# Kernel optimization log

Hardware: AMD Instinct MI355X
Metric: run time of the kernel (lower is better)

## Reference

```python
import jax, jax.numpy as jnp
import numpy as np

GROUPS = 2
EPS = 1e-5


def channel_shuffle(x, groups=2):
    b, c, h, w = x.shape
    x = x.reshape(b, groups, c // groups, h, w)
    x = jnp.transpose(x, (0, 2, 1, 3, 4))
    return x.reshape(b, c, h, w)


def binarize_weight(w):
    # w: (O, I/g, k, k). scaling_factor = mean |w| over (in,kh,kw), detached.
    scale = jax.lax.stop_gradient(jnp.mean(jnp.abs(w), axis=(1, 2, 3), keepdims=True))
    bw = scale * jnp.sign(w)
    cl = jnp.clip(w, -1.0, 1.0)
    # STE: forward value = bw, gradient flows through clamp
    return jax.lax.stop_gradient(bw) - jax.lax.stop_gradient(cl) + cl


@jax.custom_vjp
def bin_act(x):
    return jnp.sign(x)


def _bin_act_fwd(x):
    return jnp.sign(x), x


def _bin_act_bwd(x, g):
    scale = jnp.where((x >= 1.0) | (x <= -1.0), 0.01, 1.0)
    return (g * scale,)


bin_act.defvjp(_bin_act_fwd, _bin_act_bwd)


def grouped_bin_conv(x, w, pad):
    return jax.lax.conv_general_dilated(
        x, binarize_weight(w), window_strides=(1, 1),
        padding=[(pad, pad), (pad, pad)],
        dimension_numbers=('NCHW', 'OIHW', 'NCHW'),
        feature_group_count=GROUPS)


def batchnorm(x, gamma, beta):
    # training-mode BN: biased batch statistics over (N,H,W)
    mu = jnp.mean(x, axis=(0, 2, 3), keepdims=True)
    var = jnp.mean((x - mu) ** 2, axis=(0, 2, 3), keepdims=True)
    xn = (x - mu) * jax.lax.rsqrt(var + EPS)
    return xn * gamma[None, :, None, None] + beta[None, :, None, None]


def add_bias(x, b):
    return x + b[None, :, None, None]


def prelu(x, a):
    return jnp.where(x >= 0, x, a[None, :, None, None] * x)


def setup_inputs() -> dict:
    key = jax.random.key(0)
    ks = jax.random.split(key, 4)
    C, half = 256, 128
    x = jax.random.normal(ks[0], (32, C, 56, 56), dtype=jnp.float32)
    # two BinaryConvs (64,128,3,3) stacked -> grouped (128,128,3,3)
    w3 = jax.random.uniform(ks[1], (half, C // GROUPS, 3, 3), dtype=jnp.float32) * 0.001
    w1 = jax.random.uniform(ks[2], (half, C // GROUPS, 1, 1), dtype=jnp.float32) * 0.001
    z = jnp.zeros((C,), jnp.float32)
    return {
        'x': x, 'w3': w3, 'w1': w1,
        'b1': z, 'g1': jnp.ones((half,), jnp.float32), 'be1': jnp.zeros((half,), jnp.float32),
        'b2_1': z, 'a2': jnp.full((C,), 0.25, jnp.float32), 'b2_2': z,
        'b3_1': z, 'g3': jnp.ones((half,), jnp.float32), 'be3': jnp.zeros((half,), jnp.float32),
        'b4_1': z, 'a4': jnp.full((C,), 0.25, jnp.float32), 'b4_2': z,
    }


def reference(x, w3, w1, b1, g1, be1, b2_1, a2, b2_2, b3_1, g3, be3, b4_1, a4, b4_2):
    half = w3.shape[0]  # out_channel // 2 = 128
    x = channel_shuffle(x, GROUPS)
    x1 = bin_act(add_bias(x, b1))
    x1 = batchnorm(grouped_bin_conv(x1, w3, pad=1), g1, be1)
    x1_res = x[:, half:]
    x1 = x1 + x[:, :half]
    x2 = jnp.concatenate([x1, x1_res], axis=1)
    x2 = add_bias(prelu(add_bias(x2, b2_1), a2), b2_2)
    x2 = add_bias(x2, b3_1)
    x3 = bin_act(x2)
    x3 = batchnorm(grouped_bin_conv(x3, w1, pad=0), g3, be3)
    x3_res = x2[:, half:]
    x3 = x3 + x2[:, :half]
    x4 = jnp.concatenate([x3, x3_res], axis=1)
    x5 = add_bias(prelu(add_bias(x4, b4_1), a4), b4_2)
    return x5
```

## Files before the change

### kernel.cpp

```cpp
#include <hip/hip_runtime.h>
#include <stdint.h>

typedef unsigned short ushort_t;
typedef unsigned int uint_t;
typedef _Float16 half_t;

typedef float  float4_t __attribute__((ext_vector_type(4)));
typedef float  float2_t __attribute__((ext_vector_type(2)));
typedef _Float16 half4_t __attribute__((ext_vector_type(4)));
typedef _Float16 half2_t __attribute__((ext_vector_type(2)));
typedef uint_t uint4_t  __attribute__((ext_vector_type(4)));

#define B_N 32
#define C_N 256
#define HALF_N 128
#define H_N 56
#define W_N 56
#define HW_N 3136
#define NPIX (B_N * HW_N)
#define EPS_D 1e-5
#define W3S 40
#define PWS 16

__global__ void prep_kernel(const float* __restrict__ w3, const float* __restrict__ w1,
                            uint_t* __restrict__ wbits3, uint_t* __restrict__ wbits1,
                            uint_t* __restrict__ popcw3,
                            double* __restrict__ scale3, double* __restrict__ scale1,
                            double* __restrict__ sums1, double* __restrict__ sums2,
                            uint_t* __restrict__ oflags) {
    __shared__ double red[128];
    __shared__ int ipw[2][9];
    __shared__ int flsh[2];
    int t = threadIdx.x;
    int blk = blockIdx.x;
    int lane = t & 63;
    int wv = t >> 6;
    if (blk == 0) {
        sums1[t] = 0.0; sums1[128 + t] = 0.0;
        sums2[t] = 0.0; sums2[128 + t] = 0.0;
    }
    if (blk < 128) {
        int o = blk;
        double acc = 0.0;
        int anynp = 0;
        #pragma unroll
        for (int j = 0; j < 9; ++j) {
            float v = w3[o * 1152 + t * 9 + j];
            acc += fabs((double)v);
            anynp |= (v <= 0.f) ? 1 : 0;
            unsigned long long b = __ballot(v > 0.f);
            if (lane == 0) {
                wbits3[o * W3S + j * 4 + wv * 2 + 0] = (uint_t)b;
                wbits3[o * W3S + j * 4 + wv * 2 + 1] = (uint_t)(b >> 32);
                ipw[wv][j] = __popcll(b);
            }
        }
        unsigned long long m = __ballot(anynp != 0);
        if (lane == 0) flsh[wv] = (m != 0ull) ? 1 : 0;
        red[t] = acc; __syncthreads();
        for (int s = 64; s > 0; s >>= 1) { if (t < s) red[t] += red[t + s]; __syncthreads(); }
        if (t == 0) { scale3[o] = red[0] / 1152.0; oflags[o] = (uint_t)(flsh[0] | flsh[1]); }
        if (t < 9) popcw3[o * PWS + t] = (uint_t)(ipw[0][t] + ipw[1][t]);
    } else {
        int o = blk - 128;
        float v = w1[o * 128 + t];
        unsigned long long b = __ballot(v > 0.f);
        unsigned long long m = __ballot(v <= 0.f);
        if (lane == 0) {
            wbits1[o * 8 + wv * 2 + 0] = (uint_t)b;
            wbits1[o * 8 + wv * 2 + 1] = (uint_t)(b >> 32);
            flsh[wv] = (m != 0ull) ? 1 : 0;
        }
        red[t] = fabs((double)v); __syncthreads();
        for (int s = 64; s > 0; s >>= 1) { if (t < s) red[t] += red[t + s]; __syncthreads(); }
        if (t == 0) { scale1[o] = red[0] / 128.0; oflags[128 + o] = (uint_t)(flsh[0] | flsh[1]); }
    }
}

__global__ __launch_bounds__(256) void sign1_kernel(const float* __restrict__ x,
                                                    const float* __restrict__ b1,
                                                    uint_t* __restrict__ vb,
                                                    const uint_t* __restrict__ oflags,
                                                    uint_t* __restrict__ fin) {
    __shared__ int fl[4];
    int t = threadIdx.x;
    if (blockIdx.x == 0 && blockIdx.y == 0) {
        int lane = t & 63, wv4 = t >> 6;
        uint_t f = oflags[t];
        unsigned long long m = __ballot(f != 0u);
        if (lane == 0) fl[wv4] = (m != 0ull) ? 1 : 0;
        __syncthreads();
        if (t == 0) { fin[0] = (uint_t)(fl[0] | fl[1]); fin[1] = (uint_t)(fl[2] | fl[3]); }
    }
    int p = blockIdx.x * 1024 + t * 4;
    int cb = blockIdx.y * 32;
    int b = p / HW_N;
    int hw = p - b * HW_N;
    const float* xb = x + (size_t)b * C_N * HW_N + hw;
    uint_t w0 = 0, w1 = 0, w2 = 0, w3 = 0;
    #pragma unroll
    for (int j = 0; j < 32; ++j) {
        int c = cb + j;
        int src = ((c & 1) << 7) + (c >> 1);
        float4_t xv = *(const float4_t*)(xb + (size_t)src * HW_N);
        double bc = (double)b1[c];
        if ((double)xv[0] + bc > 0.0) w0 |= (1u << j);
        if ((double)xv[1] + bc > 0.0) w1 |= (1u << j);
        if ((double)xv[2] + bc > 0.0) w2 |= (1u << j);
        if ((double)xv[3] + bc > 0.0) w3 |= (1u << j);
    }
    uint4_t o4; o4[0] = w0; o4[1] = w1; o4[2] = w2; o4[3] = w3;
    *(uint4_t*)(vb + (size_t)(cb >> 5) * NPIX + p) = o4;
}

__global__ __launch_bounds__(256) void conv3_kernel(const uint_t* __restrict__ vb,
                                                    const uint_t* __restrict__ wbits3,
                                                    const uint_t* __restrict__ popcw3,
                                                    half_t* __restrict__ yh,
                                                    double* __restrict__ sums,
                                                    const uint_t* __restrict__ fin) {
    __shared__ short dlds[32][258];
    __shared__ int partS[8][32];
    __shared__ int partS2[8][32];
    int t = threadIdx.x;
    int lane = t & 63;
    int wv = t >> 6;
    bool fast = (fin[0] == 0u);
    int yb = blockIdx.y;
    if (fast && (yb & 1)) return;
    int g = yb >> 1;
    int oh = yb & 1;
    int o0 = g * 64 + oh * 32;
    int p = blockIdx.x * 256 + t;
    int hw = p % HW_N;
    int h = hw / W_N;
    int w = hw - h * W_N;
    const uint_t* vbase = vb + (size_t)g * 4 * NPIX;

    uint_t v[9][4];
    int inv[9];
    int nvalid = 0;
    #pragma unroll
    for (int j = 0; j < 9; ++j) {
        int kh = j / 3 - 1, kw = j - (j / 3) * 3 - 1;
        int hh = h + kh, ww = w + kw;
        bool valid = (hh >= 0) && (hh < H_N) && (ww >= 0) && (ww < W_N);
        inv[j] = valid ? 0 : 1;
        nvalid += valid ? 1 : 0;
        int off = p + kh * W_N + kw;
        #pragma unroll
        for (int q = 0; q < 4; ++q)
            v[j][q] = valid ? vbase[(size_t)q * NPIX + off] : 0u;
    }
    int base = 128 * nvalid;

    if (fast) {
        int P = 0;
        #pragma unroll
        for (int j = 0; j < 9; ++j)
            #pragma unroll
            for (int q = 0; q < 4; ++q)
                P += __popc(v[j][q]);
        int dot = 2 * P - base;
        yh[(size_t)o0 * NPIX + p] = (half_t)(float)dot;
        int s = dot, s2 = dot * dot;
        #pragma unroll
        for (int off = 32; off > 0; off >>= 1) {
            s  += __shfl_xor(s, off);
            s2 += __shfl_xor(s2, off);
        }
        if (lane == 0) { partS[0][wv] = s; partS2[0][wv] = s2; }
        __syncthreads();
        if (t == 0) {
            partS[1][0]  = partS[0][0] + partS[0][1] + partS[0][2] + partS[0][3];
            partS2[1][0] = partS2[0][0] + partS2[0][1] + partS2[0][2] + partS2[0][3];
        }
        __syncthreads();
        if (t < 64) {
            atomicAdd(&sums[o0 + t], (double)partS[1][0]);
            atomicAdd(&sums[128 + o0 + t], (double)partS2[1][0]);
        }
        return;
    }

    half_t* yrow = yh + (size_t)o0 * NPIX + p;
    for (int oi = 0; oi < 32; ++oi) {
        const uint_t* wo = wbits3 + (size_t)(o0 + oi) * W3S;
        const uint_t* pw = popcw3 + (size_t)(o0 + oi) * PWS;
        int acc = 0;
        #pragma unroll
        for (int j = 0; j < 9; ++j)
            #pragma unroll
            for (int q = 0; q < 4; ++q)
                acc += __popc(v[j][q] ^ wo[j * 4 + q]);
        int corr = 0;
        #pragma unroll
        for (int j = 0; j < 9; ++j) corr += inv[j] * (int)pw[j];
        int dot = base - 2 * (acc - corr);
        yrow[(size_t)oi * NPIX] = (half_t)(float)dot;
        dlds[oi][t] = (short)dot;
    }
    __syncthreads();
    {
        int o = t & 31, seg = t >> 5;
        const int* r32 = (const int*)(&dlds[o][seg * 32]);
        int S = 0, S2 = 0;
        #pragma unroll
        for (int j = 0; j < 16; ++j) {
            int pr = r32[j];
            int d0 = (int)(short)(pr & 0xffff);
            int d1 = pr >> 16;
            S += d0 + d1; S2 += d0 * d0 + d1 * d1;
        }
        partS[seg][o] = S; partS2[seg][o] = S2;
    }
    __syncthreads();
    if (t < 32) {
        int S = 0, S2 = 0;
        #pragma unroll
        for (int s8 = 0; s8 < 8; ++s8) { S += partS[s8][t]; S2 += partS2[s8][t]; }
        int c = o0 + t;
        atomicAdd(&sums[c], (double)S);
        atomicAdd(&sums[128 + c], (double)S2);
    }
}

__device__ __forceinline__ void coef_entry(const double* __restrict__ sums,
                                           const double* __restrict__ scale,
                                           const float* __restrict__ gamma,
                                           const float* __restrict__ beta,
                                           int c, double* coefL) {
    double M = (double)NPIX;
    double mean = sums[c] / M;
    double var = sums[128 + c] / M - mean * mean;
    double s = scale[c];
    double r = 1.0 / sqrt(s * s * var + EPS_D);
    double g = (double)gamma[c];
    coefL[c] = s * r * g;
    coefL[128 + c] = (double)beta[c] - s * mean * r * g;
}

__device__ __forceinline__ void coef_entry_f(const double* __restrict__ sums,
                                             const double* __restrict__ scale,
                                             const float* __restrict__ gamma,
                                             const float* __restrict__ beta,
                                             int c, float* cf) {
    double M = (double)NPIX;
    double mean = sums[c] / M;
    double var = sums[128 + c] / M - mean * mean;
    double s = scale[c];
    double r = 1.0 / sqrt(s * s * var + EPS_D);
    double g = (double)gamma[c];
    cf[c] = (float)(s * r * g);
    cf[128 + c] = (float)((double)beta[c] - s * mean * r * g);
}

__device__ __forceinline__ double x2_val(double xs, double K, bool hasy,
                                         const double* coef1, int c,
                                         const float* __restrict__ b2_1, const float* __restrict__ a2,
                                         const float* __restrict__ b2_2, const float* __restrict__ b3_1) {
    int ci = c & 127;
    double t = hasy ? (coef1[ci] * K + coef1[128 + ci] + xs) : xs;
    t += (double)b2_1[c];
    double a = (double)a2[c];
    t = (t >= 0.0) ? t : a * t;
    t += (double)b2_2[c];
    t += (double)b3_1[c];
    return t;
}

__global__ __launch_bounds__(128) void x2c1_kernel(
        const float* __restrict__ x, const half_t* __restrict__ y1h,
        const double* __restrict__ sums1, const double* __restrict__ scale3,
        const float* __restrict__ g1, const float* __restrict__ be1,
        const float* __restrict__ b2_1, const float* __restrict__ a2,
        const float* __restrict__ b2_2, const float* __restrict__ b3_1,
        const uint_t* __restrict__ wbits1,
        half_t* __restrict__ y3h, double* __restrict__ sums2,
        const float* __restrict__ b4_1, const float* __restrict__ a4,
        const float* __restrict__ b4_2, float* __restrict__ out,
        const uint_t* __restrict__ fin) {
    __shared__ double coefL[256];
    __shared__ short dst[32][258];
    __shared__ int partS[4][32];
    __shared__ int partS2[4][32];
    int t = threadIdx.x;
    int lane = t & 63;
    int wv = t >> 6;
    int g = blockIdx.y;
    bool fast3 = (fin[0] == 0u);
    bool fast1 = (fin[1] == 0u);
    if (g == 0) coef_entry(sums1, scale3, g1, be1, t, coefL);
    __syncthreads();

    int p = blockIdx.x * 256 + t * 2;
    int b = p / HW_N;
    int hw = p - b * HW_N;
    const float* xb = x + (size_t)b * C_N * HW_N + hw;

    uint_t q0 = 0, q1 = 0, q2 = 0, q3 = 0;
    uint_t r0 = 0, r1 = 0, r2 = 0, r3 = 0;
    if (g == 0) {
        if (fast3) {
            half2_t k0  = *(const half2_t*)(y1h + p);
            half2_t k64 = *(const half2_t*)(y1h + (size_t)64 * NPIX + p);
            double K0a = (double)(float)k0[0],  K0b = (double)(float)k0[1];
            double K6a = (double)(float)k64[0], K6b = (double)(float)k64[1];
            #pragma unroll
            for (int wq = 0; wq < 4; ++wq) {
                uint_t ba = 0, bb = 0;
                double Ka = (wq < 2) ? K0a : K6a;
                double Kb = (wq < 2) ? K0b : K6b;
                #pragma unroll
                for (int j = 0; j < 32; ++j) {
                    int c = wq * 32 + j;
                    int src = ((c & 1) << 7) + (c >> 1);
                    float2_t xv = *(const float2_t*)(xb + (size_t)src * HW_N);
                    double va = x2_val((double)xv[0], Ka, true, coefL, c, b2_1, a2, b2_2, b3_1);
                    double vb_ = x2_val((double)xv[1], Kb, true, coefL, c, b2_1, a2, b2_2, b3_1);
                    ba |= (va > 0.0) ? (1u << j) : 0u;
                    bb |= (vb_ > 0.0) ? (1u << j) : 0u;
                }
                if (wq == 0) { q0 = ba; r0 = bb; } else if (wq == 1) { q1 = ba; r1 = bb; }
                else if (wq == 2) { q2 = ba; r2 = bb; } else { q3 = ba; r3 = bb; }
            }
        } else {
            #pragma unroll
            for (int wq = 0; wq < 4; ++wq) {
                uint_t ba = 0, bb = 0;
                #pragma unroll
                for (int j = 0; j < 32; ++j) {
                    int c = wq * 32 + j;
                    int src = ((c & 1) << 7) + (c >> 1);
                    float2_t xv = *(const float2_t*)(xb + (size_t)src * HW_N);
                    half2_t kv = *(const half2_t*)(y1h + (size_t)c * NPIX + p);
                    double va = x2_val((double)xv[0], (double)(float)kv[0], true, coefL, c, b2_1, a2, b2_2, b3_1);
                    double vb_ = x2_val((double)xv[1], (double)(float)kv[1], true, coefL, c, b2_1, a2, b2_2, b3_1);
                    ba |= (va > 0.0) ? (1u << j) : 0u;
                    bb |= (vb_ > 0.0) ? (1u << j) : 0u;
                }
                if (wq == 0) { q0 = ba; r0 = bb; } else if (wq == 1) { q1 = ba; r1 = bb; }
                else if (wq == 2) { q2 = ba; r2 = bb; } else { q3 = ba; r3 = bb; }
            }
        }
    } else {
        #pragma unroll
        for (int wq = 0; wq < 4; ++wq) {
            uint_t ba = 0, bb = 0;
            #pragma unroll
            for (int j = 0; j < 32; ++j) {
                int c = 128 + wq * 32 + j;
                int src = ((c & 1) << 7) + (c >> 1);
                float2_t xv = *(const float2_t*)(xb + (size_t)src * HW_N);
                double va = x2_val((double)xv[0], 0.0, false, coefL, c, b2_1, a2, b2_2, b3_1);
                double vb_ = x2_val((double)xv[1], 0.0, false, coefL, c, b2_1, a2, b2_2, b3_1);
                ba |= (va > 0.0) ? (1u << j) : 0u;
                bb |= (vb_ > 0.0) ? (1u << j) : 0u;
                float b41c = b4_1[c], a4c = a4[c], b42c = b4_2[c];
                float f0 = (float)va + b41c;
                f0 = (f0 >= 0.f) ? f0 : a4c * f0;
                f0 += b42c;
                float f1 = (float)vb_ + b41c;
                f1 = (f1 >= 0.f) ? f1 : a4c * f1;
                f1 += b42c;
                float2_t ov; ov[0] = f0; ov[1] = f1;
                *(float2_t*)(out + ((size_t)b * C_N + c) * HW_N + hw) = ov;
            }
            if (wq == 0) { q0 = ba; r0 = bb; } else if (wq == 1) { q1 = ba; r1 = bb; }
            else if (wq == 2) { q2 = ba; r2 = bb; } else { q3 = ba; r3 = bb; }
        }
    }

    int obase = g * 64;
    if (fast1) {
        int P0 = __popc(q0) + __popc(q1) + __popc(q2) + __popc(q3);
        int P1 = __popc(r0) + __popc(r1) + __popc(r2) + __popc(r3);
        int d0 = 2 * P0 - 128, d1 = 2 * P1 - 128;
        half2_t yv; yv[0] = (half_t)(float)d0; yv[1] = (half_t)(float)d1;
        *(half2_t*)(y3h + (size_t)obase * NPIX + p) = yv;
        int s = d0 + d1, s2 = d0 * d0 + d1 * d1;
        #pragma unroll
        for (int off = 32; off > 0; off >>= 1) {
            s  += __shfl_xor(s, off);
            s2 += __shfl_xor(s2, off);
        }
        if (lane == 0) { partS[0][wv] = s; partS2[0][wv] = s2; }
        __syncthreads();
        if (t == 0) {
            partS[1][0]  = partS[0][0] + partS[0][1];
            partS2[1][0] = partS2[0][0] + partS2[0][1];
        }
        __syncthreads();
        if (t < 64) {
            atomicAdd(&sums2[obase + t], (double)partS[1][0]);
            atomicAdd(&sums2[128 + obase + t], (double)partS2[1][0]);
        }
        return;
    }

    #pragma unroll
    for (int ch = 0; ch < 2; ++ch) {
        #pragma unroll
        for (int oi = 0; oi < 32; ++oi) {
            int o = obase + ch * 32 + oi;
            const uint_t* wo = wbits1 + (size_t)o * 8;
            int a0 = __popc(q0 ^ wo[0]) + __popc(q1 ^ wo[1])
                   + __popc(q2 ^ wo[2]) + __popc(q3 ^ wo[3]);
            int a1 = __popc(r0 ^ wo[0]) + __popc(r1 ^ wo[1])
                   + __popc(r2 ^ wo[2]) + __popc(r3 ^ wo[3]);
            int d0 = 128 - 2 * a0, d1 = 128 - 2 * a1;
            half2_t yv; yv[0] = (half_t)(float)d0; yv[1] = (half_t)(float)d1;
            *(half2_t*)(y3h + (size_t)o * NPIX + p) = yv;
            *(int*)&dst[oi][t * 2] = (d0 & 0xffff) | (d1 << 16);
        }
        __syncthreads();
        {
            int o = t & 31, seg = t >> 5;
            const int* r32 = (const int*)(&dst[o][seg * 64]);
            int S = 0, S2 = 0;
            #pragma unroll
            for (int j = 0; j < 32; ++j) {
                int pr = r32[j];
                int e0 = (int)(short)(pr & 0xffff);
                int e1 = pr >> 16;
                S += e0 + e1; S2 += e0 * e0 + e1 * e1;
            }
            partS[seg][o] = S; partS2[seg][o] = S2;
        }
        __syncthreads();
        if (t < 32) {
            int S  = partS[0][t] + partS[1][t] + partS[2][t] + partS[3][t];
            int S2 = partS2[0][t] + partS2[1][t] + partS2[2][t] + partS2[3][t];
            int c = obase + ch * 32 + t;
            atomicAdd(&sums2[c], (double)S);
            atomicAdd(&sums2[128 + c], (double)S2);
        }
        __syncthreads();
    }
}

__global__ __launch_bounds__(256) void out_kernel(
        const float* __restrict__ x, const half_t* __restrict__ y1h,
        const half_t* __restrict__ y3h,
        const double* __restrict__ sums1, const double* __restrict__ scale3,
        const float* __restrict__ g1, const float* __restrict__ be1,
        const double* __restrict__ sums2, const double* __restrict__ scale1,
        const float* __restrict__ g3, const float* __restrict__ be3,
        const float* __restrict__ b2_1, const float* __restrict__ a2,
        const float* __restrict__ b2_2, const float* __restrict__ b3_1,
        const float* __restrict__ b4_1, const float* __restrict__ a4,
        const float* __restrict__ b4_2, float* __restrict__ out,
        const uint_t* __restrict__ fin) {
    __shared__ float c1f[256];
    __shared__ float c3f[256];
    int t = threadIdx.x;
    if (t < 128) coef_entry_f(sums1, scale3, g1, be1, t, c1f);
    else coef_entry_f(sums2, scale1, g3, be3, t - 128, c3f);
    __syncthreads();
    int c = blockIdx.y;
    int src = ((c & 1) << 7) + (c >> 1);
    int y1slice = (fin[0] == 0u) ? ((c < 64) ? 0 : 64) : c;
    int y3slice = (fin[1] == 0u) ? ((c < 64) ? 0 : 64) : c;
    float b21 = b2_1[c], aa2v = a2[c], b23 = b2_2[c] + b3_1[c];
    float b41 = b4_1[c], aa4v = a4[c], b42 = b4_2[c];
    float c1 = c1f[c], c1b = c1f[128 + c];
    float c3 = c3f[c], c3b = c3f[128 + c];
    const half_t* y1p = y1h + (size_t)y1slice * NPIX;
    const half_t* y3p = y3h + (size_t)y3slice * NPIX;
    #pragma unroll
    for (int i = 0; i < 2; ++i) {
        int p = blockIdx.x * 2048 + i * 1024 + t * 4;
        int b = p / HW_N;
        int hw = p - b * HW_N;
        float4_t xs = *(const float4_t*)(x + ((size_t)b * C_N + src) * HW_N + hw);
        half4_t y1v = *(const half4_t*)(y1p + p);
        half4_t y3v = *(const half4_t*)(y3p + p);
        float4_t ov;
        #pragma unroll
        for (int k = 0; k < 4; ++k) {
            float v = fmaf(c1, (float)y1v[k], c1b) + xs[k];
            v += b21;
            v = (v >= 0.f) ? v : aa2v * v;
            v += b23;
            float t2 = v;
            v = fmaf(c3, (float)y3v[k], c3b) + t2;
            v += b41;
            v = (v >= 0.f) ? v : aa4v * v;
            v += b42;
            ov[k] = v;
        }
        *(float4_t*)(out + ((size_t)b * C_N + c) * HW_N + hw) = ov;
    }
}

extern "C" void kernel_launch(void* const* d_in, const int* in_sizes, int n_in,
                              void* d_out, int out_size, void* d_ws, size_t ws_size,
                              hipStream_t stream) {
    const float* x    = (const float*)d_in[0];
    const float* w3   = (const float*)d_in[1];
    const float* w1   = (const float*)d_in[2];
    const float* b1   = (const float*)d_in[3];
    const float* g1   = (const float*)d_in[4];
    const float* be1  = (const float*)d_in[5];
    const float* b2_1 = (const float*)d_in[6];
    const float* a2   = (const float*)d_in[7];
    const float* b2_2 = (const float*)d_in[8];
    const float* b3_1 = (const float*)d_in[9];
    const float* g3   = (const float*)d_in[10];
    const float* be3  = (const float*)d_in[11];
    const float* b4_1 = (const float*)d_in[12];
    const float* a4   = (const float*)d_in[13];
    const float* b4_2 = (const float*)d_in[14];

    char* ws = (char*)d_ws;
    half_t* y1h    = (half_t*)(ws + 0);
    half_t* y3h    = (half_t*)(ws + 25690112);
    uint_t* wbits3 = (uint_t*)(ws + 51380224);
    uint_t* wbits1 = (uint_t*)(ws + 51400704);
    uint_t* popcw3 = (uint_t*)(ws + 51404800);
    double* scale3 = (double*)(ws + 51412992);
    double* scale1 = (double*)(ws + 51414016);
    double* sums1  = (double*)(ws + 51415040);
    double* sums2  = (double*)(ws + 51417088);
    uint_t* oflags = (uint_t*)(ws + 51419136);
    uint_t* fin    = (uint_t*)(ws + 51420160);

    uint_t* vb1 = (uint_t*)((char*)d_out + 0);
    float*  outp = (float*)d_out;

    prep_kernel<<<256, 128, 0, stream>>>(w3, w1, wbits3, wbits1, popcw3,
                                         scale3, scale1, sums1, sums2, oflags);
    sign1_kernel<<<dim3(NPIX / 1024, 8), 256, 0, stream>>>(x, b1, vb1, oflags, fin);
    conv3_kernel<<<dim3(NPIX / 256, 4), 256, 0, stream>>>(vb1, wbits3, popcw3, y1h, sums1, fin);
    x2c1_kernel<<<dim3(NPIX / 256, 2), 128, 0, stream>>>(x, y1h, sums1, scale3, g1, be1,
                                                         b2_1, a2, b2_2, b3_1,
                                                         wbits1, y3h, sums2,
                                                         b4_1, a4, b4_2, outp, fin);
    out_kernel<<<dim3(NPIX / 2048, 128), 256, 0, stream>>>(x, y1h, y3h,
                                                           sums1, scale3, g1, be1,
                                                           sums2, scale1, g3, be3,
                                                           b2_1, a2, b2_2, b3_1,
                                                           b4_1, a4, b4_2, outp, fin);
}
```

Baseline: 288.0 us.

## Halve per-thread pixel work in sign and x2c1 kernels, split channels across threads

sign1_kernel now handles two pixels per thread with float2 loads, doubling the grid. x2c1_kernel processes one pixel per thread and splits the 128 input channels between two thread halves, exchanging the bit words through shared memory, using 256 threads and twice as many blocks. The aim is more parallelism and latency hiding in these bandwidth-bound kernels. In exchange, global accesses become narrower scalar loads and stores, and the kernel adds a shared-memory exchange and an extra barrier.

```diff
diff --git a/kernel.cpp b/kernel.cpp
--- a/kernel.cpp
+++ b/kernel.cpp
@@ -10,6 +10,7 @@
 typedef _Float16 half4_t __attribute__((ext_vector_type(4)));
 typedef _Float16 half2_t __attribute__((ext_vector_type(2)));
 typedef uint_t uint4_t  __attribute__((ext_vector_type(4)));
+typedef uint_t uint2_t  __attribute__((ext_vector_type(2)));
 
 #define B_N 32
 #define C_N 256
@@ -92,25 +93,23 @@
         __syncthreads();
         if (t == 0) { fin[0] = (uint_t)(fl[0] | fl[1]); fin[1] = (uint_t)(fl[2] | fl[3]); }
     }
-    int p = blockIdx.x * 1024 + t * 4;
+    int p = blockIdx.x * 512 + t * 2;
     int cb = blockIdx.y * 32;
     int b = p / HW_N;
     int hw = p - b * HW_N;
     const float* xb = x + (size_t)b * C_N * HW_N + hw;
-    uint_t w0 = 0, w1 = 0, w2 = 0, w3 = 0;
+    uint_t w0 = 0, w1 = 0;
     #pragma unroll
     for (int j = 0; j < 32; ++j) {
         int c = cb + j;
         int src = ((c & 1) << 7) + (c >> 1);
-        float4_t xv = *(const float4_t*)(xb + (size_t)src * HW_N);
+        float2_t xv = *(const float2_t*)(xb + (size_t)src * HW_N);
         double bc = (double)b1[c];
         if ((double)xv[0] + bc > 0.0) w0 |= (1u << j);
         if ((double)xv[1] + bc > 0.0) w1 |= (1u << j);
-        if ((double)xv[2] + bc > 0.0) w2 |= (1u << j);
-        if ((double)xv[3] + bc > 0.0) w3 |= (1u << j);
-    }
-    uint4_t o4; o4[0] = w0; o4[1] = w1; o4[2] = w2; o4[3] = w3;
-    *(uint4_t*)(vb + (size_t)(cb >> 5) * NPIX + p) = o4;
+    }
+    uint2_t o2; o2[0] = w0; o2[1] = w1;
+    *(uint2_t*)(vb + (size_t)(cb >> 5) * NPIX + p) = o2;
 }
 
 __global__ __launch_bounds__(256) void conv3_kernel(const uint_t* __restrict__ vb,
@@ -269,7 +268,7 @@
     return t;
 }
 
-__global__ __launch_bounds__(128) void x2c1_kernel(
+__global__ __launch_bounds__(256) void x2c1_kernel(
         const float* __restrict__ x, const half_t* __restrict__ y1h,
         const double* __restrict__ sums1, const double* __restrict__ scale3,
         const float* __restrict__ g1, const float* __restrict__ be1,
@@ -281,110 +280,99 @@
         const float* __restrict__ b4_2, float* __restrict__ out,
         const uint_t* __restrict__ fin) {
     __shared__ double coefL[256];
-    __shared__ short dst[32][258];
-    __shared__ int partS[4][32];
-    __shared__ int partS2[4][32];
+    __shared__ uint_t shW[128][5];
+    __shared__ short dst[64][130];
+    __shared__ int partS[4][64];
+    __shared__ int partS2[4][64];
     int t = threadIdx.x;
     int lane = t & 63;
     int wv = t >> 6;
+    int pl = t & 127;
+    int ch = t >> 7;
     int g = blockIdx.y;
     bool fast3 = (fin[0] == 0u);
     bool fast1 = (fin[1] == 0u);
-    if (g == 0) coef_entry(sums1, scale3, g1, be1, t, coefL);
-    __syncthreads();
-
-    int p = blockIdx.x * 256 + t * 2;
+    if (g == 0 && t < 128) coef_entry(sums1, scale3, g1, be1, t, coefL);
+    __syncthreads();
+
+    int p = blockIdx.x * 128 + pl;
     int b = p / HW_N;
     int hw = p - b * HW_N;
     const float* xb = x + (size_t)b * C_N * HW_N + hw;
 
-    uint_t q0 = 0, q1 = 0, q2 = 0, q3 = 0;
-    uint_t r0 = 0, r1 = 0, r2 = 0, r3 = 0;
+    uint_t wA = 0, wB = 0;
     if (g == 0) {
         if (fast3) {
-            half2_t k0  = *(const half2_t*)(y1h + p);
-            half2_t k64 = *(const half2_t*)(y1h + (size_t)64 * NPIX + p);
-            double K0a = (double)(float)k0[0],  K0b = (double)(float)k0[1];
-            double K6a = (double)(float)k64[0], K6b = (double)(float)k64[1];
+            double K = (double)(float)y1h[(size_t)(ch * 64) * NPIX + p];
             #pragma unroll
-            for (int wq = 0; wq < 4; ++wq) {
-                uint_t ba = 0, bb = 0;
-                double Ka = (wq < 2) ? K0a : K6a;
-                double Kb = (wq < 2) ? K0b : K6b;
+            for (int wq = 0; wq < 2; ++wq) {
+                uint_t bits = 0u;
                 #pragma unroll
                 for (int j = 0; j < 32; ++j) {
-                    int c = wq * 32 + j;
+                    int c = ch * 64 + wq * 32 + j;
                     int src = ((c & 1) << 7) + (c >> 1);
-                    float2_t xv = *(const float2_t*)(xb + (size_t)src * HW_N);
-                    double va = x2_val((double)xv[0], Ka, true, coefL, c, b2_1, a2, b2_2, b3_1);
-                    double vb_ = x2_val((double)xv[1], Kb, true, coefL, c, b2_1, a2, b2_2, b3_1);
-                    ba |= (va > 0.0) ? (1u << j) : 0u;
-                    bb |= (vb_ > 0.0) ? (1u << j) : 0u;
+                    double xs = (double)xb[(size_t)src * HW_N];
+                    double v = x2_val(xs, K, true, coefL, c, b2_1, a2, b2_2, b3_1);
+                    bits |= (v > 0.0) ? (1u << j) : 0u;
                 }
-                if (wq == 0) { q0 = ba; r0 = bb; } else if (wq == 1) { q1 = ba; r1 = bb; }
-                else if (wq == 2) { q2 = ba; r2 = bb; } else { q3 = ba; r3 = bb; }
+                if (wq == 0) wA = bits; else wB = bits;
             }
         } else {
             #pragma unroll
-            for (int wq = 0; wq < 4; ++wq) {
-                uint_t ba = 0, bb = 0;
+            for (int wq = 0; wq < 2; ++wq) {
+                uint_t bits = 0u;
                 #pragma unroll
                 for (int j = 0; j < 32; ++j) {
-                    int c = wq * 32 + j;
+                    int c = ch * 64 + wq * 32 + j;
                     int src = ((c & 1) << 7) + (c >> 1);
-                    float2_t xv = *(const float2_t*)(xb + (size_t)src * HW_N);
-                    half2_t kv = *(const half2_t*)(y1h + (size_t)c * NPIX + p);
-                    double va = x2_val((double)xv[0], (double)(float)kv[0], true, coefL, c, b2_1, a2, b2_2, b3_1);
-                    double vb_ = x2_val((double)xv[1], (double)(float)kv[1], true, coefL, c, b2_1, a2, b2_2, b3_1);
-                    ba |= (va > 0.0) ? (1u << j) : 0u;
-                    bb |= (vb_ > 0.0) ? (1u << j) : 0u;
+                    double xs = (double)xb[(size_t)src * HW_N];
+                    double K = (double)(float)y1h[(size_t)c * NPIX + p];
+                    double v = x2_val(xs, K, true, coefL, c, b2_1, a2, b2_2, b3_1);
+                    bits |= (v > 0.0) ? (1u << j) : 0u;
                 }
-                if (wq == 0) { q0 = ba; r0 = bb; } else if (wq == 1) { q1 = ba; r1 = bb; }
-                else if (wq == 2) { q2 = ba; r2 = bb; } else { q3 = ba; r3 = bb; }
+                if (wq == 0) wA = bits; else wB = bits;
             }
         }
     } else {
         #pragma unroll
-        for (int wq = 0; wq < 4; ++wq) {
-            uint_t ba = 0, bb = 0;
+        for (int wq = 0; wq < 2; ++wq) {
+            uint_t bits = 0u;
             #pragma unroll
             for (int j = 0; j < 32; ++j) {
-                int c = 128 + wq * 32 + j;
+                int c = 128 + ch * 64 + wq * 32 + j;
                 int src = ((c & 1) << 7) + (c >> 1);
-                float2_t xv = *(const float2_t*)(xb + (size_t)src * HW_N);
-                double va = x2_val((double)xv[0], 0.0, false, coefL, c, b2_1, a2, b2_2, b3_1);
-                double vb_ = x2_val((double)xv[1], 0.0, false, coefL, c, b2_1, a2, b2_2, b3_1);
-                ba |= (va > 0.0) ? (1u << j) : 0u;
-                bb |= (vb_ > 0.0) ? (1u << j) : 0u;
+                double xs = (double)xb[(size_t)src * HW_N];
+                double v = x2_val(xs, 0.0, false, coefL, c, b2_1, a2, b2_2, b3_1);
+                bits |= (v > 0.0) ? (1u << j) : 0u;
                 float b41c = b4_1[c], a4c = a4[c], b42c = b4_2[c];
-                float f0 = (float)va + b41c;
+                float f0 = (float)v + b41c;
                 f0 = (f0 >= 0.f) ? f0 : a4c * f0;
                 f0 += b42c;
-                float f1 = (float)vb_ + b41c;
-                f1 = (f1 >= 0.f) ? f1 : a4c * f1;
-                f1 += b42c;
-                float2_t ov; ov[0] = f0; ov[1] = f1;
-                *(float2_t*)(out + ((size_t)b * C_N + c) * HW_N + hw) = ov;
+                out[((size_t)b * C_N + c) * HW_N + hw] = f0;
             }
-            if (wq == 0) { q0 = ba; r0 = bb; } else if (wq == 1) { q1 = ba; r1 = bb; }
-            else if (wq == 2) { q2 = ba; r2 = bb; } else { q3 = ba; r3 = bb; }
-        }
-    }
+            if (wq == 0) wA = bits; else wB = bits;
+        }
+    }
+
+    shW[pl][2 * ch + 0] = wA;
+    shW[pl][2 * ch + 1] = wB;
+    __syncthreads();
+    uint_t W0 = shW[pl][0], W1 = shW[pl][1], W2 = shW[pl][2], W3 = shW[pl][3];
 
     int obase = g * 64;
     if (fast1) {
-        int P0 = __popc(q0) + __popc(q1) + __popc(q2) + __popc(q3);
-        int P1 = __popc(r0) + __popc(r1) + __popc(r2) + __popc(r3);
-        int d0 = 2 * P0 - 128, d1 = 2 * P1 - 128;
-        half2_t yv; yv[0] = (half_t)(float)d0; yv[1] = (half_t)(float)d1;
-        *(half2_t*)(y3h + (size_t)obase * NPIX + p) = yv;
-        int s = d0 + d1, s2 = d0 * d0 + d1 * d1;
-        #pragma unroll
-        for (int off = 32; off > 0; off >>= 1) {
-            s  += __shfl_xor(s, off);
-            s2 += __shfl_xor(s2, off);
-        }
-        if (lane == 0) { partS[0][wv] = s; partS2[0][wv] = s2; }
+        if (ch == 0) {
+            int P = __popc(W0) + __popc(W1) + __popc(W2) + __popc(W3);
+            int dot = 2 * P - 128;
+            y3h[(size_t)obase * NPIX + p] = (half_t)(float)dot;
+            int s = dot, s2 = dot * dot;
+            #pragma unroll
+            for (int off = 32; off > 0; off >>= 1) {
+                s  += __shfl_xor(s, off);
+                s2 += __shfl_xor(s2, off);
+            }
+            if (lane == 0) { partS[0][wv] = s; partS2[0][wv] = s2; }
+        }
         __syncthreads();
         if (t == 0) {
             partS[1][0]  = partS[0][0] + partS[0][1];
@@ -399,43 +387,36 @@
     }
 
     #pragma unroll
-    for (int ch = 0; ch < 2; ++ch) {
-        #pragma unroll
-        for (int oi = 0; oi < 32; ++oi) {
-            int o = obase + ch * 32 + oi;
-            const uint_t* wo = wbits1 + (size_t)o * 8;
-            int a0 = __popc(q0 ^ wo[0]) + __popc(q1 ^ wo[1])
-                   + __popc(q2 ^ wo[2]) + __popc(q3 ^ wo[3]);
-            int a1 = __popc(r0 ^ wo[0]) + __popc(r1 ^ wo[1])
-                   + __popc(r2 ^ wo[2]) + __popc(r3 ^ wo[3]);
-            int d0 = 128 - 2 * a0, d1 = 128 - 2 * a1;
-            half2_t yv; yv[0] = (half_t)(float)d0; yv[1] = (half_t)(float)d1;
-            *(half2_t*)(y3h + (size_t)o * NPIX + p) = yv;
-            *(int*)&dst[oi][t * 2] = (d0 & 0xffff) | (d1 << 16);
-        }
-        __syncthreads();
-        {
-            int o = t & 31, seg = t >> 5;
-            const int* r32 = (const int*)(&dst[o][seg * 64]);
-            int S = 0, S2 = 0;
-            #pragma unroll
-            for (int j = 0; j < 32; ++j) {
-                int pr = r32[j];
-                int e0 = (int)(short)(pr & 0xffff);
-                int e1 = pr >> 16;
-                S += e0 + e1; S2 += e0 * e0 + e1 * e1;
-            }
-            partS[seg][o] = S; partS2[seg][o] = S2;
-        }
-        __syncthreads();
-        if (t < 32) {
-            int S  = partS[0][t] + partS[1][t] + partS[2][t] + partS[3][t];
-            int S2 = partS2[0][t] + partS2[1][t] + partS2[2][t] + partS2[3][t];
-            int c = obase + ch * 32 + t;
-            atomicAdd(&sums2[c], (double)S);
-            atomicAdd(&sums2[128 + c], (double)S2);
-        }
-        __syncthreads();
+    for (int oi = 0; oi < 32; ++oi) {
+        int o = obase + ch * 32 + oi;
+        const uint_t* wo = wbits1 + (size_t)o * 8;
+        int acc = __popc(W0 ^ wo[0]) + __popc(W1 ^ wo[1])
+                + __popc(W2 ^ wo[2]) + __popc(W3 ^ wo[3]);
+        int dot = 128 - 2 * acc;
+        y3h[(size_t)o * NPIX + p] = (half_t)(float)dot;
+        dst[ch * 32 + oi][pl] = (short)dot;
+    }
+    __syncthreads();
+    {
+        int o = t & 63, seg = t >> 6;
+        const int* r32 = (const int*)(&dst[o][seg * 32]);
+        int S = 0, S2 = 0;
+        #pragma unroll
+        for (int j = 0; j < 16; ++j) {
+            int pr = r32[j];
+            int e0 = (int)(short)(pr & 0xffff);
+            int e1 = pr >> 16;
+            S += e0 + e1; S2 += e0 * e0 + e1 * e1;
+        }
+        partS[seg][o] = S; partS2[seg][o] = S2;
+    }
+    __syncthreads();
+    if (t < 64) {
+        int S  = partS[0][t] + partS[1][t] + partS[2][t] + partS[3][t];
+        int S2 = partS2[0][t] + partS2[1][t] + partS2[2][t] + partS2[3][t];
+        int c = obase + t;
+        atomicAdd(&sums2[c], (double)S);
+        atomicAdd(&sums2[128 + c], (double)S2);
     }
 }
 
@@ -530,9 +511,9 @@
 
     prep_kernel<<<256, 128, 0, stream>>>(w3, w1, wbits3, wbits1, popcw3,
                                          scale3, scale1, sums1, sums2, oflags);
-    sign1_kernel<<<dim3(NPIX / 1024, 8), 256, 0, stream>>>(x, b1, vb1, oflags, fin);
+    sign1_kernel<<<dim3(NPIX / 512, 8), 256, 0, stream>>>(x, b1, vb1, oflags, fin);
     conv3_kernel<<<dim3(NPIX / 256, 4), 256, 0, stream>>>(vb1, wbits3, popcw3, y1h, sums1, fin);
-    x2c1_kernel<<<dim3(NPIX / 256, 2), 128, 0, stream>>>(x, y1h, sums1, scale3, g1, be1,
+    x2c1_kernel<<<dim3(NPIX / 128, 2), 256, 0, stream>>>(x, y1h, sums1, scale3, g1, be1,
                                                          b2_1, a2, b2_2, b3_1,
                                                          wbits1, y3h, sums2,
                                                          b4_1, a4, b4_2, outp, fin);
```

After: 314.1 us. 1.09x slower.
